# Kernel tuning notes

Hardware: AMD Instinct MI355X
Metric: run time of the kernel (lower is better)

The kernel has to match this reference:

```python
import jax, jax.numpy as jnp
import numpy as np

B, S, I, H, L, O = 64, 1024, 128, 512, 3, 128


def _linear_w(key, shape, fan_in):
    # mimic nn.Linear default init: U(-1/sqrt(fan_in), 1/sqrt(fan_in))
    bound = 1.0 / np.sqrt(fan_in)
    return jax.random.uniform(key, shape, jnp.float32, -bound, bound)


def setup_inputs() -> dict:
    key = jax.random.key(0)
    ks = jax.random.split(key, 20)
    inp = {
        "input": jax.random.normal(ks[0], (B, S, I), jnp.float32),
        "hidden_state": jnp.zeros((B, L, H), jnp.float32),
        # layer-0 input->hidden gate weights (no bias), in_features = I
        "Wx0z": _linear_w(ks[1], (H, I), I),
        "Wx0r": _linear_w(ks[2], (H, I), I),
        "Wx0g": _linear_w(ks[3], (H, I), I),
        # layers 1..L-1 input->hidden gate weights (no bias), in_features = H
        "Wxz": _linear_w(ks[4], (L - 1, H, H), H),
        "Wxr": _linear_w(ks[5], (L - 1, H, H), H),
        "Wxg": _linear_w(ks[6], (L - 1, H, H), H),
        # hidden->hidden gate weights + biases, all layers
        "Whz": _linear_w(ks[7], (L, H, H), H),
        "Whr": _linear_w(ks[8], (L, H, H), H),
        "Whg": _linear_w(ks[9], (L, H, H), H),
        "bz": _linear_w(ks[10], (L, H), H),
        "br": _linear_w(ks[11], (L, H), H),
        "bg": _linear_w(ks[12], (L, H), H),
        # output projection
        "Wy": _linear_w(ks[13], (O, H), H),
        "by": _linear_w(ks[14], (O,), H),
    }
    return inp


def reference(input, hidden_state, Wx0z, Wx0r, Wx0g, Wxz, Wxr, Wxg,
              Whz, Whr, Whg, bz, br, bg, Wy, by):
    # dropout p=0 -> identity
    def step(h, x_t):  # h: (L,B,H), x_t: (B,I)
        x = x_t
        new_h = []
        for i in range(L):
            wxz = Wx0z if i == 0 else Wxz[i - 1]
            wxr = Wx0r if i == 0 else Wxr[i - 1]
            wxg = Wx0g if i == 0 else Wxg[i - 1]
            hi = h[i]
            z = jax.nn.sigmoid(hi @ Whz[i].T + bz[i] + x @ wxz.T)
            r = jax.nn.sigmoid(hi @ Whr[i].T + br[i] + x @ wxr.T)
            g = jnp.tanh((r * hi) @ Whg[i].T + bg[i] + x @ wxg.T)
            hn = z * hi + (1.0 - z) * g
            new_h.append(hn)
            x = hn
        y = x @ Wy.T + by  # (B,O)
        return jnp.stack(new_h), y

    h0 = jnp.transpose(hidden_state, (1, 0, 2))  # (L,B,H)
    xs = jnp.transpose(input, (1, 0, 2))         # (S,B,I)
    h_final, ys = jax.lax.scan(step, h0, xs)
    layer_output = jnp.transpose(ys, (1, 0, 2))      # (B,S,O)
    hidden_out = jnp.transpose(h_final, (1, 0, 2))   # (B,L,H)
    return layer_output, hidden_out
```

## Files before the change

kernel.cpp:

```cpp
#include <hip/hip_runtime.h>


typedef float f32x4 __attribute__((ext_vector_type(4)));
typedef __bf16 bf16x8 __attribute__((ext_vector_type(8)));

#define CT 128
#define NCHUNK 8
#define CC 32
#define POIS 0x7FC07FC0
#define PSLOT_SHORTS 12582912ull
#define PGATE_BYTES  8388608ull
#define USLOT_SHORTS 4194304ull

struct RecMeta {
  int l[3];
  int ts[3];
  int slot[3];
};

__device__ __forceinline__ unsigned short f2bf(float x) {
  unsigned int u = __builtin_bit_cast(unsigned int, x);
  u += 0x7fffu + ((u >> 16) & 1u);
  return (unsigned short)(u >> 16);
}
__device__ __forceinline__ float bf2f(unsigned short h) {
  unsigned int u = ((unsigned int)h) << 16;
  return __builtin_bit_cast(float, u);
}
__device__ __forceinline__ f32x4 mfma16(int4 a, int4 b, f32x4 c) {
  return __builtin_amdgcn_mfma_f32_16x16x32_bf16(
      __builtin_bit_cast(bf16x8, a), __builtin_bit_cast(bf16x8, b), c, 0, 0, 0);
}
__device__ __forceinline__ float sig_(float x) { return 1.0f / (1.0f + __expf(-x)); }
__device__ __forceinline__ float tanh_(float x) {
  float ax = fabsf(x);
  float e  = __expf(2.0f * ax);
  float t  = 1.0f - 2.0f / (e + 1.0f);
  return x < 0.0f ? -t : t;
}

__device__ __forceinline__ void issue_ld16(const unsigned short* p, int4& d) {
  asm volatile("global_load_dwordx4 %0, %1, off sc0 sc1"
               : "=v"(d) : "v"(p) : "memory");
}
__device__ __forceinline__ void st_wt128(unsigned short* p, int4 v) {
  unsigned long long lo = ((unsigned long long)(unsigned int)v.y << 32) | (unsigned int)v.x;
  unsigned long long hi = ((unsigned long long)(unsigned int)v.w << 32) | (unsigned int)v.z;
  __hip_atomic_store((unsigned long long*)p,     lo, __ATOMIC_RELAXED, __HIP_MEMORY_SCOPE_AGENT);
  __hip_atomic_store((unsigned long long*)p + 1, hi, __ATOMIC_RELAXED, __HIP_MEMORY_SCOPE_AGENT);
}
__device__ __forceinline__ void wait_vm0() {
  asm volatile("s_waitcnt vmcnt(0)" ::: "memory");
}

__device__ __forceinline__ void poll_slab16(const unsigned short* p, int4* d) {
  for (;;) {
#pragma unroll
    for (int kc = 0; kc < 16; kc++) issue_ld16(p + kc * 32, d[kc]);
    wait_vm0();
    int bad = 0;
#pragma unroll
    for (int kc = 0; kc < 16; kc++)
      bad |= (d[kc].x == POIS) | (d[kc].y == POIS) | (d[kc].z == POIS) | (d[kc].w == POIS);
    if (!__any(bad)) return;
  }
}

__global__ void cvt_bf16(const float* __restrict__ src, unsigned short* __restrict__ dst, int n4) {
  int i = blockIdx.x * blockDim.x + threadIdx.x;
  if (i < n4) {
    float4 v = *(const float4*)(src + (size_t)i * 4);
    ushort4 o;
    o.x = f2bf(v.x); o.y = f2bf(v.y); o.z = f2bf(v.z); o.w = f2bf(v.w);
    *(ushort4*)(dst + (size_t)i * 4) = o;
  }
}

__global__ void xt_k(const float* __restrict__ X, unsigned short* __restrict__ Xt) {
  int idx = blockIdx.x * 256 + threadIdx.x;
  int i4 = idx & 31, rest = idx >> 5;
  int t = rest & 1023, b = rest >> 10;
  float4 v = *(const float4*)(X + (size_t)(b * 1024 + t) * 128 + i4 * 4);
  ushort4 o;
  o.x = f2bf(v.x); o.y = f2bf(v.y); o.z = f2bf(v.z); o.w = f2bf(v.w);
  *(ushort4*)(Xt + (size_t)(t * 64 + b) * 128 + i4 * 4) = o;
}

__global__ void poison_k(unsigned long long* __restrict__ a,
                         unsigned long long* __restrict__ b) {
  const unsigned long long P = 0x7FC07FC07FC07FC0ull;
  unsigned long long* pa = a + (size_t)blockIdx.x * 1024 + threadIdx.x;
  unsigned long long* pb = b + (size_t)blockIdx.x * 1024 + threadIdx.x;
#pragma unroll
  for (int k = 0; k < 4; k++) {
    __hip_atomic_store(pa + k * 256, P, __ATOMIC_RELAXED, __HIP_MEMORY_SCOPE_AGENT);
    __hip_atomic_store(pb + k * 256, P, __ATOMIC_RELAXED, __HIP_MEMORY_SCOPE_AGENT);
  }
}

__global__ __launch_bounds__(256)
void gemm3(const unsigned short* __restrict__ A,
           const unsigned short* __restrict__ Wz, const unsigned short* __restrict__ Wr,
           const unsigned short* __restrict__ Wg,
           unsigned short* __restrict__ Pz, unsigned short* __restrict__ Pr,
           unsigned short* __restrict__ Pg,
           int M, int K) {
  __shared__ unsigned short As[128][72];
  __shared__ unsigned short Bs[128][72];
  const int gate = blockIdx.y >> 2;
  const unsigned short* W = (gate == 0) ? Wz : (gate == 1) ? Wr : Wg;
  unsigned short* C       = (gate == 0) ? Pz : (gate == 1) ? Pr : Pg;
  const int tid  = threadIdx.x;
  const int lane = tid & 63;
  const int wave = tid >> 6;
  const int wr = wave >> 1, wc = wave & 1;
  const int m0 = blockIdx.x * 128, n0 = (blockIdx.y & 3) * 128;

  f32x4 acc[4][4];
  for (int i = 0; i < 4; i++)
    for (int j = 0; j < 4; j++) acc[i][j] = f32x4{0.f, 0.f, 0.f, 0.f};

  for (int k0 = 0; k0 < K; k0 += 64) {
    int4 va[4], vb[4];
#pragma unroll
    for (int it = 0; it < 4; it++) {
      int q = tid + it * 256;
      int r = q >> 3, kc = q & 7;
      va[it] = *(const int4*)(A + (size_t)(m0 + r) * K + k0 + kc * 8);
      vb[it] = *(const int4*)(W + (size_t)(n0 + r) * K + k0 + kc * 8);
    }
    __syncthreads();
#pragma unroll
    for (int it = 0; it < 4; it++) {
      int q = tid + it * 256;
      int r = q >> 3, kc = q & 7;
      *(int4*)&As[r][kc * 8] = va[it];
      *(int4*)&Bs[r][kc * 8] = vb[it];
    }
    __syncthreads();
#pragma unroll
    for (int kc = 0; kc < 2; kc++) {
      int koff = kc * 32 + (lane >> 4) * 8;
      int4 af[4], bfr[4];
#pragma unroll
      for (int mt = 0; mt < 4; mt++) af[mt]  = *(const int4*)&As[wr * 64 + mt * 16 + (lane & 15)][koff];
#pragma unroll
      for (int nt = 0; nt < 4; nt++) bfr[nt] = *(const int4*)&Bs[wc * 64 + nt * 16 + (lane & 15)][koff];
#pragma unroll
      for (int mt = 0; mt < 4; mt++)
#pragma unroll
        for (int nt = 0; nt < 4; nt++)
          acc[mt][nt] = mfma16(af[mt], bfr[nt], acc[mt][nt]);
    }
  }

#pragma unroll
  for (int mt = 0; mt < 4; mt++)
#pragma unroll
    for (int nt = 0; nt < 4; nt++)
#pragma unroll
      for (int rg = 0; rg < 4; rg++) {
        int m = m0 + wr * 64 + mt * 16 + (lane >> 4) * 4 + rg;
        int n = n0 + wc * 64 + nt * 16 + (lane & 15);
        C[(size_t)m * 512 + n] = f2bf(acc[mt][nt][rg]);
      }
}

__global__ __launch_bounds__(256)
void gemm_bt(const unsigned short* __restrict__ A, const unsigned short* __restrict__ W,
             float* __restrict__ Cout, const float* __restrict__ bias,
             int M, int N, int K) {
  __shared__ unsigned short As[128][72];
  __shared__ unsigned short Bs[128][72];
  const int tid  = threadIdx.x;
  const int lane = tid & 63;
  const int wave = tid >> 6;
  const int wr = wave >> 1, wc = wave & 1;
  const int m0 = blockIdx.x * 128, n0 = blockIdx.y * 128;

  f32x4 acc[4][4];
  for (int i = 0; i < 4; i++)
    for (int j = 0; j < 4; j++) acc[i][j] = f32x4{0.f, 0.f, 0.f, 0.f};

  for (int k0 = 0; k0 < K; k0 += 64) {
    int4 va[4], vb[4];
#pragma unroll
    for (int it = 0; it < 4; it++) {
      int q = tid + it * 256;
      int r = q >> 3, kc = q & 7;
      va[it] = *(const int4*)(A + (size_t)(m0 + r) * K + k0 + kc * 8);
      vb[it] = *(const int4*)(W + (size_t)(n0 + r) * K + k0 + kc * 8);
    }
    __syncthreads();
#pragma unroll
    for (int it = 0; it < 4; it++) {
      int q = tid + it * 256;
      int r = q >> 3, kc = q & 7;
      *(int4*)&As[r][kc * 8] = va[it];
      *(int4*)&Bs[r][kc * 8] = vb[it];
    }
    __syncthreads();
#pragma unroll
    for (int kc = 0; kc < 2; kc++) {
      int koff = kc * 32 + (lane >> 4) * 8;
      int4 af[4], bfr[4];
#pragma unroll
      for (int mt = 0; mt < 4; mt++) af[mt]  = *(const int4*)&As[wr * 64 + mt * 16 + (lane & 15)][koff];
#pragma unroll
      for (int nt = 0; nt < 4; nt++) bfr[nt] = *(const int4*)&Bs[wc * 64 + nt * 16 + (lane & 15)][koff];
#pragma unroll
      for (int mt = 0; mt < 4; mt++)
#pragma unroll
        for (int nt = 0; nt < 4; nt++)
          acc[mt][nt] = mfma16(af[mt], bfr[nt], acc[mt][nt]);
    }
  }

#pragma unroll
  for (int mt = 0; mt < 4; mt++)
#pragma unroll
    for (int nt = 0; nt < 4; nt++)
#pragma unroll
      for (int rg = 0; rg < 4; rg++) {
        int m = m0 + wr * 64 + mt * 16 + (lane >> 4) * 4 + rg;
        int n = n0 + wc * 64 + nt * 16 + (lane & 15);
        Cout[(size_t)((m & 63) * 1024 + (m >> 6)) * N + n] = acc[mt][nt][rg] + bias[n];
      }
}

__global__ __launch_bounds__(128)
void gru_rec(const float* __restrict__ Whz, const float* __restrict__ Whr,
             const float* __restrict__ Whg,
             const float* __restrict__ bz, const float* __restrict__ br,
             const float* __restrict__ bg,
             const unsigned short* __restrict__ PzB, const unsigned short* __restrict__ PrB,
             const unsigned short* __restrict__ PgB,
             const float* __restrict__ h0,
             float* __restrict__ hstateB,
             unsigned short* __restrict__ Hbuf,
             unsigned short* __restrict__ UbufB,
             float* __restrict__ hidout,
             RecMeta meta) {
  const int cell = blockIdx.x >> 6;
  const int bid  = blockIdx.x & 63;
  const int layer  = meta.l[cell];
  const int tstart = meta.ts[cell];
  const int slot   = meta.slot[cell];
  const unsigned short* Pz = PzB + (size_t)slot * PSLOT_SHORTS;
  const unsigned short* Pr = PrB + (size_t)slot * PSLOT_SHORTS;
  const unsigned short* Pg = PgB + (size_t)slot * PSLOT_SHORTS;
  unsigned short* Ubuf     = UbufB + (size_t)slot * USLOT_SHORTS;
  float* hstate            = hstateB + (size_t)layer * 32768;

  const int g    = bid & 3;
  const int mem  = bid >> 2;
  const int cbase = mem * CC;
  const int tid  = threadIdx.x;
  const int lane = tid & 63;
  const int wave = tid >> 6;

  __shared__ unsigned short Whs[3][64][32][8];
  __shared__ float hloc[16][CC + 1];
  __shared__ float zbuf[16][CC + 1];
  __shared__ unsigned short un[16][40];
  __shared__ unsigned short hnew[16][40];

  {
    const float* wsrc[3] = { Whz + (size_t)layer * 262144,
                             Whr + (size_t)layer * 262144,
                             Whg + (size_t)layer * 262144 };
    for (int idx = tid; idx < 12288; idx += 128) {
      int gate = idx >> 12;
      int r = idx & 4095;
      int c = r >> 7, k4 = r & 127;
      float4 v = *(const float4*)(wsrc[gate] + (size_t)(cbase + c) * 512 + k4 * 4);
      int o = k4 >> 1, base = (k4 & 1) * 4;
      Whs[gate][o][c][base + 0] = f2bf(v.x);
      Whs[gate][o][c][base + 1] = f2bf(v.y);
      Whs[gate][o][c][base + 2] = f2bf(v.z);
      Whs[gate][o][c][base + 3] = f2bf(v.w);
    }
  }
  for (int q = tid; q < 16 * CC; q += 128) {
    int row = q >> 5, c = q & 31;
    int b = g * 16 + row;
    hloc[row][c] = (tstart == 0)
                     ? h0[(size_t)b * 1536 + layer * 512 + cbase + c]
                     : hstate[(size_t)b * 512 + cbase + c];
  }
  __syncthreads();

  const int l15 = lane & 15;
  const int kq  = lane >> 4;

  float bzc[2], brc[2], bgc[2];
#pragma unroll
  for (int T = 0; T < 2; T++) {
    bzc[T] = bz[(size_t)layer * 512 + cbase + T * 16 + l15];
    brc[T] = br[(size_t)layer * 512 + cbase + T * 16 + l15];
    bgc[T] = bg[(size_t)layer * 512 + cbase + T * 16 + l15];
  }

  for (int tl = 0; tl < CT; tl++) {
    if (wave == 0) {
      float pr[2][4], pz[2][4];
#pragma unroll
      for (int T = 0; T < 2; T++)
#pragma unroll
        for (int rg = 0; rg < 4; rg++) {
          size_t off = (size_t)tl * 32768 + (size_t)(g * 16 + kq * 4 + rg) * 512 + cbase + T * 16 + l15;
          pr[T][rg] = bf2f(Pr[off]);
          pz[T][rg] = bf2f(Pz[off]);
        }
      int4 hf[16];
      if (tl == 0) {
        const float* hs = (tstart == 0)
                            ? h0 + (size_t)(g * 16 + l15) * 1536 + (size_t)layer * 512
                            : hstate + (size_t)(g * 16 + l15) * 512;
#pragma unroll
        for (int kc = 0; kc < 16; kc++) {
          int c0 = kq * 8 + kc * 32;
          float4 v0 = *(const float4*)(hs + c0);
          float4 v1 = *(const float4*)(hs + c0 + 4);
          int w0 = (int)f2bf(v0.x) | ((int)f2bf(v0.y) << 16);
          int w1 = (int)f2bf(v0.z) | ((int)f2bf(v0.w) << 16);
          int w2 = (int)f2bf(v1.x) | ((int)f2bf(v1.y) << 16);
          int w3 = (int)f2bf(v1.z) | ((int)f2bf(v1.w) << 16);
          hf[kc] = int4{w0, w1, w2, w3};
        }
      } else {
        poll_slab16(Hbuf + (size_t)(tstart + tl - 1) * 32768 + (g * 16 + l15) * 512 + kq * 8, hf);
      }
      f32x4 ar[2] = { f32x4{0.f,0.f,0.f,0.f}, f32x4{0.f,0.f,0.f,0.f} };
#pragma unroll
      for (int kc = 0; kc < 16; kc++)
#pragma unroll
        for (int T = 0; T < 2; T++)
          ar[T] = mfma16(hf[kc], *(const int4*)&Whs[1][kc * 4 + kq][T * 16 + l15][0], ar[T]);
#pragma unroll
      for (int T = 0; T < 2; T++)
#pragma unroll
        for (int rg = 0; rg < 4; rg++) {
          int row = kq * 4 + rg, c = T * 16 + l15;
          float rv = sig_(ar[T][rg] + pr[T][rg] + brc[T]);
          un[row][c] = f2bf(rv * hloc[row][c]);
        }
      {
        int4 v = *(const int4*)&un[lane >> 2][(lane & 3) * 8];
        st_wt128(Ubuf + (size_t)tl * 32768 + (g * 16 + (lane >> 2)) * 512 + cbase + (lane & 3) * 8, v);
      }
      f32x4 az[2] = { f32x4{0.f,0.f,0.f,0.f}, f32x4{0.f,0.f,0.f,0.f} };
#pragma unroll
      for (int kc = 0; kc < 16; kc++)
#pragma unroll
        for (int T = 0; T < 2; T++)
          az[T] = mfma16(hf[kc], *(const int4*)&Whs[0][kc * 4 + kq][T * 16 + l15][0], az[T]);
#pragma unroll
      for (int T = 0; T < 2; T++)
#pragma unroll
        for (int rg = 0; rg < 4; rg++)
          zbuf[kq * 4 + rg][T * 16 + l15] = sig_(az[T][rg] + pz[T][rg] + bzc[T]);
    } else {
      float pg[2][4];
#pragma unroll
      for (int T = 0; T < 2; T++)
#pragma unroll
        for (int rg = 0; rg < 4; rg++)
          pg[T][rg] = bf2f(Pg[(size_t)tl * 32768 + (size_t)(g * 16 + kq * 4 + rg) * 512 + cbase + T * 16 + l15]);
      int4 uf[16];
      poll_slab16(Ubuf + (size_t)tl * 32768 + (g * 16 + l15) * 512 + kq * 8, uf);
      f32x4 ag[2] = { f32x4{0.f,0.f,0.f,0.f}, f32x4{0.f,0.f,0.f,0.f} };
#pragma unroll
      for (int kc = 0; kc < 16; kc++)
#pragma unroll
        for (int T = 0; T < 2; T++)
          ag[T] = mfma16(uf[kc], *(const int4*)&Whs[2][kc * 4 + kq][T * 16 + l15][0], ag[T]);
#pragma unroll
      for (int T = 0; T < 2; T++)
#pragma unroll
        for (int rg = 0; rg < 4; rg++)
          ag[T][rg] += pg[T][rg] + bgc[T];
      __syncthreads();
#pragma unroll
      for (int T = 0; T < 2; T++)
#pragma unroll
        for (int rg = 0; rg < 4; rg++) {
          int row = kq * 4 + rg, c = T * 16 + l15;
          float gv = tanh_(ag[T][rg]);
          float z  = zbuf[row][c];
          float h  = hloc[row][c];
          float hn = z * h + (1.0f - z) * gv;
          hloc[row][c] = hn;
          hnew[row][c] = f2bf(hn);
        }
      {
        int4 v = *(const int4*)&hnew[lane >> 2][(lane & 3) * 8];
        st_wt128(&Hbuf[(size_t)(tstart + tl) * 32768 + (g * 16 + (lane >> 2)) * 512 + cbase + (lane & 3) * 8], v);
      }
    }
    if (wave == 0) __syncthreads();
    __syncthreads();
  }

  for (int q = tid; q < 16 * CC; q += 128) {
    int row = q >> 5, c = q & 31;
    int b = g * 16 + row;
    float v = hloc[row][c];
    hstate[(size_t)b * 512 + cbase + c] = v;
    if (tstart + CT == 1024)
      hidout[(size_t)b * 1536 + layer * 512 + cbase + c] = v;
  }
}

extern "C" void kernel_launch(void* const* d_in, const int* in_sizes, int n_in,
                              void* d_out, int out_size, void* d_ws, size_t ws_size,
                              hipStream_t stream) {
  const float* X    = (const float*)d_in[0];
  const float* H0   = (const float*)d_in[1];
  const float* Wx0z = (const float*)d_in[2];
  const float* Wx0r = (const float*)d_in[3];
  const float* Wx0g = (const float*)d_in[4];
  const float* Wxz  = (const float*)d_in[5];
  const float* Wxr  = (const float*)d_in[6];
  const float* Wxg  = (const float*)d_in[7];
  const float* Whz  = (const float*)d_in[8];
  const float* Whr  = (const float*)d_in[9];
  const float* Whg  = (const float*)d_in[10];
  const float* bz   = (const float*)d_in[11];
  const float* br   = (const float*)d_in[12];
  const float* bg   = (const float*)d_in[13];
  const float* Wy   = (const float*)d_in[14];
  const float* by   = (const float*)d_in[15];

  int nslot = (ws_size >= 188612608ull) ? 3 : 1;

  char* w = (char*)d_ws;
  unsigned short* Xt    = (unsigned short*)(w + 0);
  unsigned short* Wx0zb = (unsigned short*)(w + 16777216);
  unsigned short* Wx0rb = (unsigned short*)(w + 16908288);
  unsigned short* Wx0gb = (unsigned short*)(w + 17039360);
  unsigned short* Wxzb  = (unsigned short*)(w + 17170432);
  unsigned short* Wxrb  = (unsigned short*)(w + 18219008);
  unsigned short* Wxgb  = (unsigned short*)(w + 19267584);
  unsigned short* Wyb   = (unsigned short*)(w + 20316160);
  const size_t off = 20447232;
  unsigned short* PzB = (unsigned short*)(w + off);
  unsigned short* PrB = (unsigned short*)(w + off + PGATE_BYTES);
  unsigned short* PgB = (unsigned short*)(w + off + 2 * PGATE_BYTES);
  size_t hbOff  = off + (size_t)nslot * (PSLOT_SHORTS * 2);
  unsigned short* Hb  = (unsigned short*)(w + hbOff);
  size_t hstOff = hbOff + 67108864;
  float* hst          = (float*)(w + hstOff);
  size_t uOff   = hstOff + 393216;
  unsigned short* UbB = (unsigned short*)(w + uOff);

  auto cvt = [&](const float* s, unsigned short* d, int n) {
    int n4 = n / 4;
    cvt_bf16<<<dim3((n4 + 255) / 256), dim3(256), 0, stream>>>(s, d, n4);
  };
  xt_k<<<dim3(8192), dim3(256), 0, stream>>>(X, Xt);
  cvt(Wx0z, Wx0zb, 65536);
  cvt(Wx0r, Wx0rb, 65536);
  cvt(Wx0g, Wx0gb, 65536);
  cvt(Wxz, Wxzb, 524288);
  cvt(Wxr, Wxrb, 524288);
  cvt(Wxg, Wxgb, 524288);
  cvt(Wy, Wyb, 65536);

  float* hidout = (float*)d_out + 8388608;

  static const signed char sched3[10][3] = {
      {0,-1,-1},{1,8,-1},{2,9,16},{3,10,17},{4,11,18},
      {5,12,19},{6,13,20},{7,14,21},{15,22,-1},{23,-1,-1}};
  static const signed char sched1[24][3] = {
      {0,-1,-1},{1,-1,-1},{2,-1,-1},{3,-1,-1},{4,-1,-1},{5,-1,-1},
      {6,-1,-1},{7,-1,-1},{8,-1,-1},{9,-1,-1},{10,-1,-1},{11,-1,-1},
      {12,-1,-1},{13,-1,-1},{14,-1,-1},{15,-1,-1},{16,-1,-1},{17,-1,-1},
      {18,-1,-1},{19,-1,-1},{20,-1,-1},{21,-1,-1},{22,-1,-1},{23,-1,-1}};
  const signed char (*sched)[3] = (nslot == 3) ? sched3 : sched1;
  const int ndisp = (nslot == 3) ? 10 : 24;

  for (int d = 0; d < ndisp; d++) {
    RecMeta meta{};
    int nc = 0;
    for (int s = 0; s < 3; s++) {
      int cid = sched[d][s];
      if (cid < 0) break;
      int layer = cid >> 3, chunk = cid & 7, tstart = chunk * CT;
      const unsigned short *Ap, *wz, *wr_, *wg;
      int K;
      if (layer == 0) {
        Ap = Xt + (size_t)tstart * 64 * 128;
        wz = Wx0zb; wr_ = Wx0rb; wg = Wx0gb; K = 128;
      } else {
        Ap = Hb + (size_t)tstart * 32768;
        wz = Wxzb + (size_t)(layer - 1) * 262144;
        wr_ = Wxrb + (size_t)(layer - 1) * 262144;
        wg = Wxgb + (size_t)(layer - 1) * 262144;
        K = 512;
      }
      gemm3<<<dim3(CT * 64 / 128, 12), 256, 0, stream>>>(
          Ap, wz, wr_, wg,
          PzB + (size_t)nc * PSLOT_SHORTS,
          PrB + (size_t)nc * PSLOT_SHORTS,
          PgB + (size_t)nc * PSLOT_SHORTS,
          CT * 64, K);
      meta.l[nc] = layer; meta.ts[nc] = tstart; meta.slot[nc] = nc;
      nc++;
    }
    for (int s = 0; s < nc; s++) {
      poison_k<<<dim3(1024), dim3(256), 0, stream>>>(
          (unsigned long long*)(Hb + (size_t)meta.ts[s] * 32768),
          (unsigned long long*)(UbB + (size_t)meta.slot[s] * USLOT_SHORTS));
    }
    gru_rec<<<dim3(nc * 64), dim3(128), 0, stream>>>(
        Whz, Whr, Whg, bz, br, bg, PzB, PrB, PgB, H0, hst, Hb, UbB,
        hidout, meta);
  }

  gemm_bt<<<dim3(512, 1), 256, 0, stream>>>(Hb, Wyb, (float*)d_out, by, 65536, 128, 512);
}
```

Baseline: 10.88 ms.

## Halve recurrence chunk length, pre-convert Wh to bf16, merge poison launches

The time-chunk length drops from 128 to 64 steps, doubling the number of chunks so the layer wavefront pipeline has shorter fill and drain phases. The hand-written schedule tables are replaced by a diagonal schedule computed on the host. The hidden-to-hidden weights are now converted to bf16 once, in the swizzled layout, by a new kernel, so each recurrence block only does a vectorized copy into shared memory instead of fp32 loads plus conversion. The per-cell poison launches are merged into one launch per dispatch. The trade-off is more dispatches, each with its own GEMM and recurrence launch overhead.

```diff
diff --git a/kernel.cpp b/kernel.cpp
--- a/kernel.cpp
+++ b/kernel.cpp
@@ -4,13 +4,13 @@
 typedef float f32x4 __attribute__((ext_vector_type(4)));
 typedef __bf16 bf16x8 __attribute__((ext_vector_type(8)));
 
-#define CT 128
-#define NCHUNK 8
+#define CT 64
+#define NCHUNK 16
 #define CC 32
 #define POIS 0x7FC07FC0
-#define PSLOT_SHORTS 12582912ull
-#define PGATE_BYTES  8388608ull
-#define USLOT_SHORTS 4194304ull
+#define PGATE_BYTES  4194304ull
+#define PSLOT_SHORTS 6291456ull
+#define USLOT_SHORTS 2097152ull
 
 struct RecMeta {
   int l[3];
@@ -86,16 +86,40 @@
   *(ushort4*)(Xt + (size_t)(t * 64 + b) * 128 + i4 * 4) = o;
 }
 
-__global__ void poison_k(unsigned long long* __restrict__ a,
-                         unsigned long long* __restrict__ b) {
+__global__ void whcvt_k(const float* __restrict__ Whz, const float* __restrict__ Whr,
+                        const float* __restrict__ Whg, unsigned short* __restrict__ Whb) {
+  int layer = blockIdx.x >> 4, slice = blockIdx.x & 15;
+  const float* wsrc[3] = { Whz + (size_t)layer * 262144,
+                           Whr + (size_t)layer * 262144,
+                           Whg + (size_t)layer * 262144 };
+  unsigned short* dst = Whb + (size_t)layer * 786432 + (size_t)slice * 49152;
+  int cbase = slice * 32;
+  for (int idx = threadIdx.x; idx < 12288; idx += 256) {
+    int gate = idx >> 12, r = idx & 4095, c = r >> 7, k4 = r & 127;
+    float4 v = *(const float4*)(wsrc[gate] + (size_t)(cbase + c) * 512 + k4 * 4);
+    int o = k4 >> 1, base = (k4 & 1) * 4;
+    ushort4 out;
+    out.x = f2bf(v.x); out.y = f2bf(v.y); out.z = f2bf(v.z); out.w = f2bf(v.w);
+    *(ushort4*)(dst + gate * 16384 + o * 256 + c * 8 + base) = out;
+  }
+}
+
+__global__ void poison3_k(unsigned long long* __restrict__ hb,
+                          unsigned long long* __restrict__ ub, RecMeta meta) {
   const unsigned long long P = 0x7FC07FC07FC07FC0ull;
-  unsigned long long* pa = a + (size_t)blockIdx.x * 1024 + threadIdx.x;
-  unsigned long long* pb = b + (size_t)blockIdx.x * 1024 + threadIdx.x;
-#pragma unroll
-  for (int k = 0; k < 4; k++) {
-    __hip_atomic_store(pa + k * 256, P, __ATOMIC_RELAXED, __HIP_MEMORY_SCOPE_AGENT);
-    __hip_atomic_store(pb + k * 256, P, __ATOMIC_RELAXED, __HIP_MEMORY_SCOPE_AGENT);
-  }
+  int cell = blockIdx.x >> 9;
+  int inner = blockIdx.x & 511;
+  unsigned long long* base;
+  if (inner < 256) {
+    base = hb + (size_t)meta.ts[cell] * 8192;
+  } else {
+    base = ub + (size_t)meta.slot[cell] * (USLOT_SHORTS / 4);
+    inner -= 256;
+  }
+  unsigned long long* p = base + (size_t)inner * 2048 + threadIdx.x;
+#pragma unroll
+  for (int k = 0; k < 8; k++)
+    __hip_atomic_store(p + k * 256, P, __ATOMIC_RELAXED, __HIP_MEMORY_SCOPE_AGENT);
 }
 
 __global__ __launch_bounds__(256)
@@ -229,8 +253,7 @@
 }
 
 __global__ __launch_bounds__(128)
-void gru_rec(const float* __restrict__ Whz, const float* __restrict__ Whr,
-             const float* __restrict__ Whg,
+void gru_rec(const unsigned short* __restrict__ Whb,
              const float* __restrict__ bz, const float* __restrict__ br,
              const float* __restrict__ bg,
              const unsigned short* __restrict__ PzB, const unsigned short* __restrict__ PrB,
@@ -259,27 +282,17 @@
   const int lane = tid & 63;
   const int wave = tid >> 6;
 
-  __shared__ unsigned short Whs[3][64][32][8];
+  __shared__ __align__(16) unsigned short Whs[3][64][32][8];
   __shared__ float hloc[16][CC + 1];
   __shared__ float zbuf[16][CC + 1];
   __shared__ unsigned short un[16][40];
   __shared__ unsigned short hnew[16][40];
 
   {
-    const float* wsrc[3] = { Whz + (size_t)layer * 262144,
-                             Whr + (size_t)layer * 262144,
-                             Whg + (size_t)layer * 262144 };
-    for (int idx = tid; idx < 12288; idx += 128) {
-      int gate = idx >> 12;
-      int r = idx & 4095;
-      int c = r >> 7, k4 = r & 127;
-      float4 v = *(const float4*)(wsrc[gate] + (size_t)(cbase + c) * 512 + k4 * 4);
-      int o = k4 >> 1, base = (k4 & 1) * 4;
-      Whs[gate][o][c][base + 0] = f2bf(v.x);
-      Whs[gate][o][c][base + 1] = f2bf(v.y);
-      Whs[gate][o][c][base + 2] = f2bf(v.z);
-      Whs[gate][o][c][base + 3] = f2bf(v.w);
-    }
+    const unsigned short* src = Whb + (size_t)layer * 786432 + (size_t)mem * 49152;
+    unsigned short* ds = &Whs[0][0][0][0];
+    for (int i = tid; i < 6144; i += 128)
+      *(int4*)(ds + (size_t)i * 8) = *(const int4*)(src + (size_t)i * 8);
   }
   for (int q = tid; q < 16 * CC; q += 128) {
     int row = q >> 5, c = q & 31;
@@ -432,7 +445,7 @@
   const float* Wy   = (const float*)d_in[14];
   const float* by   = (const float*)d_in[15];
 
-  int nslot = (ws_size >= 188612608ull) ? 3 : 1;
+  int nslot = (ws_size >= 142999552ull) ? 3 : 1;
 
   char* w = (char*)d_ws;
   unsigned short* Xt    = (unsigned short*)(w + 0);
@@ -453,6 +466,8 @@
   float* hst          = (float*)(w + hstOff);
   size_t uOff   = hstOff + 393216;
   unsigned short* UbB = (unsigned short*)(w + uOff);
+  size_t whbOff = uOff + (size_t)nslot * (USLOT_SHORTS * 2);
+  unsigned short* Whb = (unsigned short*)(w + whbOff);
 
   auto cvt = [&](const float* s, unsigned short* d, int n) {
     int n4 = n / 4;
@@ -466,27 +481,26 @@
   cvt(Wxr, Wxrb, 524288);
   cvt(Wxg, Wxgb, 524288);
   cvt(Wy, Wyb, 65536);
+  whcvt_k<<<dim3(48), dim3(256), 0, stream>>>(Whz, Whr, Whg, Whb);
 
   float* hidout = (float*)d_out + 8388608;
 
-  static const signed char sched3[10][3] = {
-      {0,-1,-1},{1,8,-1},{2,9,16},{3,10,17},{4,11,18},
-      {5,12,19},{6,13,20},{7,14,21},{15,22,-1},{23,-1,-1}};
-  static const signed char sched1[24][3] = {
-      {0,-1,-1},{1,-1,-1},{2,-1,-1},{3,-1,-1},{4,-1,-1},{5,-1,-1},
-      {6,-1,-1},{7,-1,-1},{8,-1,-1},{9,-1,-1},{10,-1,-1},{11,-1,-1},
-      {12,-1,-1},{13,-1,-1},{14,-1,-1},{15,-1,-1},{16,-1,-1},{17,-1,-1},
-      {18,-1,-1},{19,-1,-1},{20,-1,-1},{21,-1,-1},{22,-1,-1},{23,-1,-1}};
-  const signed char (*sched)[3] = (nslot == 3) ? sched3 : sched1;
-  const int ndisp = (nslot == 3) ? 10 : 24;
+  const int ndisp = (nslot == 3) ? (NCHUNK + 2) : (3 * NCHUNK);
 
   for (int d = 0; d < ndisp; d++) {
     RecMeta meta{};
+    int cl[3], cch[3];
     int nc = 0;
-    for (int s = 0; s < 3; s++) {
-      int cid = sched[d][s];
-      if (cid < 0) break;
-      int layer = cid >> 3, chunk = cid & 7, tstart = chunk * CT;
+    if (nslot == 3) {
+      for (int l = 0; l < 3; l++) {
+        int c = d - l;
+        if (c >= 0 && c < NCHUNK) { cl[nc] = l; cch[nc] = c; nc++; }
+      }
+    } else {
+      cl[0] = d / NCHUNK; cch[0] = d % NCHUNK; nc = 1;
+    }
+    for (int s = 0; s < nc; s++) {
+      int layer = cl[s], tstart = cch[s] * CT;
       const unsigned short *Ap, *wz, *wr_, *wg;
       int K;
       if (layer == 0) {
@@ -501,20 +515,16 @@
       }
       gemm3<<<dim3(CT * 64 / 128, 12), 256, 0, stream>>>(
           Ap, wz, wr_, wg,
-          PzB + (size_t)nc * PSLOT_SHORTS,
-          PrB + (size_t)nc * PSLOT_SHORTS,
-          PgB + (size_t)nc * PSLOT_SHORTS,
+          PzB + (size_t)s * PSLOT_SHORTS,
+          PrB + (size_t)s * PSLOT_SHORTS,
+          PgB + (size_t)s * PSLOT_SHORTS,
           CT * 64, K);
-      meta.l[nc] = layer; meta.ts[nc] = tstart; meta.slot[nc] = nc;
-      nc++;
-    }
-    for (int s = 0; s < nc; s++) {
-      poison_k<<<dim3(1024), dim3(256), 0, stream>>>(
-          (unsigned long long*)(Hb + (size_t)meta.ts[s] * 32768),
-          (unsigned long long*)(UbB + (size_t)meta.slot[s] * USLOT_SHORTS));
-    }
+      meta.l[s] = layer; meta.ts[s] = tstart; meta.slot[s] = s;
+    }
+    poison3_k<<<dim3(nc * 512), dim3(256), 0, stream>>>(
+        (unsigned long long*)Hb, (unsigned long long*)UbB, meta);
     gru_rec<<<dim3(nc * 64), dim3(128), 0, stream>>>(
-        Whz, Whr, Whg, bz, br, bg, PzB, PrB, PgB, H0, hst, Hb, UbB,
+        Whb, bz, br, bg, PzB, PrB, PgB, H0, hst, Hb, UbB,
         hidout, meta);
   }
 
```

New measurement: 10.70 ms. About the same (-1.7%).
